# Kernel tuning notes

Measured on AMD Instinct MI355X. Metric: run time of the kernel, lower is better.

Reference implementation:

```python
import jax, jax.numpy as jnp
import numpy as np

B, L, D = 16, 2048, 1024
S = 32                      # spans per example
WIDTH_BUCKET, LEN_BUCKET = 16, 32
NUM_BUCKETS = 64
NUM_LABELS = 3


def setup_inputs() -> dict:
    key = jax.random.key(0)
    k1, k2, k3, k4, k5, k6 = jax.random.split(key, 6)
    encoder_layer = jax.random.normal(k1, (B, L, D), dtype=jnp.float32)
    # variable sequence lengths in [1024, 2048]
    lengths = jax.random.randint(k2, (B,), 1024, L + 1)
    attention_mask = (jnp.arange(L)[None, :] < lengths[:, None]).astype(jnp.int32)
    # non-overlapping spans of width 64: pooled region is [head+1, tail), never empty
    span_head_idxs = jnp.broadcast_to(jnp.arange(S, dtype=jnp.int32) * 64, (B, S))
    span_tail_idxs = span_head_idxs + 64
    labels = jax.random.randint(k3, (B, S), 0, NUM_LABELS, dtype=jnp.int32)
    width_emb = jax.random.normal(k4, (NUM_BUCKETS, 8), dtype=jnp.float32) * 0.02
    length_emb = jax.random.normal(k5, (NUM_BUCKETS, 8), dtype=jnp.float32) * 0.02
    cls_w = jax.random.normal(k6, (D + 16, NUM_LABELS), dtype=jnp.float32) * 0.02
    cls_b = jnp.zeros((NUM_LABELS,), dtype=jnp.float32)
    return {
        "encoder_layer": encoder_layer,
        "attention_mask": attention_mask,
        "span_head_idxs": span_head_idxs,
        "span_tail_idxs": span_tail_idxs,
        "labels": labels,
        "width_emb": width_emb,
        "length_emb": length_emb,
        "cls_w": cls_w,
        "cls_b": cls_b,
    }


def reference(encoder_layer, attention_mask, span_head_idxs, span_tail_idxs,
              labels, width_emb, length_emb, cls_w, cls_b):
    b, l, d = encoder_layer.shape
    s = span_head_idxs.shape[1]
    pos = jnp.arange(l, dtype=jnp.int32)  # [L]
    # ragged span mean: mean over encoder_layer[i, head+1 : tail]
    in_span = (pos[None, None, :] >= span_head_idxs[:, :, None] + 1) & \
              (pos[None, None, :] < span_tail_idxs[:, :, None])           # [B,S,L]
    m = in_span.astype(encoder_layer.dtype)
    counts = jnp.maximum(m.sum(-1, keepdims=True), 1.0)                   # [B,S,1]
    span_mean = jnp.einsum('bsl,bld->bsd', m, encoder_layer) / counts     # [B,S,D]
    # width bucket embedding
    w_bucket = jnp.clip((span_tail_idxs - span_head_idxs) // WIDTH_BUCKET, 0, NUM_BUCKETS - 1)
    width_vec = width_emb[w_bucket]                                       # [B,S,8]
    # length bucket embedding (per-example, broadcast over spans)
    lengths = attention_mask.sum(1)                                       # [B]
    l_bucket = jnp.clip(lengths // LEN_BUCKET, 0, NUM_BUCKETS - 1)
    length_vec = jnp.broadcast_to(length_emb[l_bucket][:, None, :], (b, s, length_emb.shape[1]))
    feat = jnp.concatenate([span_mean, width_vec, length_vec], axis=-1)   # [B,S,D+16]
    # dropout is identity in eval mode
    logits = feat @ cls_w + cls_b                                         # [B,S,num_labels]
    # cross-entropy with ignore_index=-1
    logp = jax.nn.log_softmax(logits, axis=-1).reshape(-1, logits.shape[-1])
    lab = labels.reshape(-1)
    valid = lab > -1
    nll = -jnp.take_along_axis(logp, jnp.clip(lab, 0)[:, None], axis=1)[:, 0]
    ce_loss = jnp.sum(jnp.where(valid, nll, 0.0)) / jnp.maximum(valid.sum(), 1)
    return logits, ce_loss
```

## Files before the change

### kernel.cpp

```cpp
#include <hip/hip_runtime.h>
#include <hip/hip_bf16.h>

#define B_ 16
#define L_ 2048
#define D_ 1024
#define S_ 32

__global__ __launch_bounds__(256) void lengths_kernel(const int* __restrict__ mask,
                                                      int* __restrict__ lbuck) {
    const int b = blockIdx.x;
    const int t = threadIdx.x;
    int s = 0;
    for (int i = t; i < L_; i += 256) s += mask[b * L_ + i];
#pragma unroll
    for (int off = 32; off > 0; off >>= 1) s += __shfl_down(s, off, 64);
    __shared__ int red[4];
    if ((t & 63) == 0) red[t >> 6] = s;
    __syncthreads();
    if (t == 0) {
        int tot = red[0] + red[1] + red[2] + red[3];
        int lb = tot / 32;
        if (lb < 0) lb = 0;
        if (lb > 63) lb = 63;
        lbuck[b] = lb;
    }
}

__global__ __launch_bounds__(256) void span_logits_kernel(
        const float* __restrict__ enc,
        const int* __restrict__ head,
        const int* __restrict__ tail,
        const float* __restrict__ wemb,
        const float* __restrict__ lemb,
        const float* __restrict__ cls_w,
        const float* __restrict__ cls_b,
        const int* __restrict__ lbuck,
        float* __restrict__ out) {
    const int bs = blockIdx.x;
    const int b  = bs / S_;
    const int t  = threadIdx.x;
    const int h  = head[bs];
    const int tl = tail[bs];
    int lo = h + 1; if (lo < 0) lo = 0;
    int hi = tl;    if (hi > L_) hi = L_;
    const int nrow = hi - lo;

    const int dc = t * 4;

    float w00 = cls_w[(dc + 0) * 3 + 0], w01 = cls_w[(dc + 0) * 3 + 1], w02 = cls_w[(dc + 0) * 3 + 2];
    float w10 = cls_w[(dc + 1) * 3 + 0], w11 = cls_w[(dc + 1) * 3 + 1], w12 = cls_w[(dc + 1) * 3 + 2];
    float w20 = cls_w[(dc + 2) * 3 + 0], w21 = cls_w[(dc + 2) * 3 + 1], w22 = cls_w[(dc + 2) * 3 + 2];
    float w30 = cls_w[(dc + 3) * 3 + 0], w31 = cls_w[(dc + 3) * 3 + 1], w32 = cls_w[(dc + 3) * 3 + 2];

    float a0 = 0.f, a1 = 0.f, a2 = 0.f;
    const float* base = enc + (size_t)b * (L_ * D_) + dc;
    for (int l = lo; l < hi; ++l) {
        const float4 u = *reinterpret_cast<const float4*>(base + (size_t)l * D_);
        a0 = fmaf(u.x, w00, a0); a1 = fmaf(u.x, w01, a1); a2 = fmaf(u.x, w02, a2);
        a0 = fmaf(u.y, w10, a0); a1 = fmaf(u.y, w11, a1); a2 = fmaf(u.y, w12, a2);
        a0 = fmaf(u.z, w20, a0); a1 = fmaf(u.z, w21, a1); a2 = fmaf(u.z, w22, a2);
        a0 = fmaf(u.w, w30, a0); a1 = fmaf(u.w, w31, a1); a2 = fmaf(u.w, w32, a2);
    }

#pragma unroll
    for (int off = 32; off > 0; off >>= 1) {
        a0 += __shfl_down(a0, off, 64);
        a1 += __shfl_down(a1, off, 64);
        a2 += __shfl_down(a2, off, 64);
    }
    __shared__ float sred[12];
    const int wv = t >> 6;
    if ((t & 63) == 0) { sred[wv * 3 + 0] = a0; sred[wv * 3 + 1] = a1; sred[wv * 3 + 2] = a2; }
    __syncthreads();

    if (t == 0) {
        float r0 = sred[0] + sred[3] + sred[6] + sred[9];
        float r1 = sred[1] + sred[4] + sred[7] + sred[10];
        float r2 = sred[2] + sred[5] + sred[8] + sred[11];
        float cnt = (float)(nrow > 0 ? nrow : 0);
        if (cnt < 1.f) cnt = 1.f;
        const float inv = 1.f / cnt;
        r0 *= inv; r1 *= inv; r2 *= inv;

        int wb = (tl - h) / 16;
        if (wb < 0) wb = 0;
        if (wb > 63) wb = 63;
        const int lb = lbuck[b];
        const float* we = wemb + wb * 8;
        const float* le = lemb + lb * 8;
#pragma unroll
        for (int j = 0; j < 8; ++j) {
            const float wvf = we[j];
            const float lvf = le[j];
            r0 += wvf * cls_w[(D_ + j) * 3 + 0] + lvf * cls_w[(D_ + 8 + j) * 3 + 0];
            r1 += wvf * cls_w[(D_ + j) * 3 + 1] + lvf * cls_w[(D_ + 8 + j) * 3 + 1];
            r2 += wvf * cls_w[(D_ + j) * 3 + 2] + lvf * cls_w[(D_ + 8 + j) * 3 + 2];
        }
        r0 += cls_b[0];
        r1 += cls_b[1];
        r2 += cls_b[2];

        out[bs * 3 + 0] = r0;
        out[bs * 3 + 1] = r1;
        out[bs * 3 + 2] = r2;
    }
}

__global__ __launch_bounds__(512) void ce_kernel(const float* __restrict__ logits,
                                                 const int* __restrict__ labels,
                                                 float* __restrict__ out) {
    const int i = threadIdx.x;
    const int lab = labels[i];
    const float l0 = logits[i * 3 + 0];
    const float l1 = logits[i * 3 + 1];
    const float l2 = logits[i * 3 + 2];
    const float m  = fmaxf(l0, fmaxf(l1, l2));
    const float lse = m + logf(expf(l0 - m) + expf(l1 - m) + expf(l2 - m));
    int cl = lab < 0 ? 0 : (lab > 2 ? 2 : lab);
    const float pick = (cl == 0) ? l0 : ((cl == 1) ? l1 : l2);
    float nll = 0.f, val = 0.f;
    if (lab > -1) { nll = lse - pick; val = 1.f; }
#pragma unroll
    for (int off = 32; off > 0; off >>= 1) {
        nll += __shfl_down(nll, off, 64);
        val += __shfl_down(val, off, 64);
    }
    __shared__ float rn[8], rv[8];
    const int wv = i >> 6;
    if ((i & 63) == 0) { rn[wv] = nll; rv[wv] = val; }
    __syncthreads();
    if (i == 0) {
        float sn = 0.f, sv = 0.f;
#pragma unroll
        for (int k = 0; k < 8; ++k) { sn += rn[k]; sv += rv[k]; }
        out[B_ * S_ * 3] = sn / fmaxf(sv, 1.f);
    }
}

extern "C" void kernel_launch(void* const* d_in, const int* in_sizes, int n_in,
                              void* d_out, int out_size, void* d_ws, size_t ws_size,
                              hipStream_t stream) {
    const float* enc    = (const float*)d_in[0];
    const int*   mask   = (const int*)d_in[1];
    const int*   head   = (const int*)d_in[2];
    const int*   tail   = (const int*)d_in[3];
    const int*   labels = (const int*)d_in[4];
    const float* wemb   = (const float*)d_in[5];
    const float* lemb   = (const float*)d_in[6];
    const float* cls_w  = (const float*)d_in[7];
    const float* cls_b  = (const float*)d_in[8];
    float* out = (float*)d_out;

    int* lbuck = (int*)d_ws;

    lengths_kernel<<<B_, 256, 0, stream>>>(mask, lbuck);
    span_logits_kernel<<<B_ * S_, 256, 0, stream>>>(enc, head, tail, wemb, lemb,
                                                    cls_w, cls_b, lbuck, out);
    ce_kernel<<<1, 512, 0, stream>>>(out, labels, out);
}
```

Measured before the change: 219.0 us.

## Fuse length reduction into span kernel and split span rows across four thread groups

Removes the separate lengths kernel: each span block now reads the example's 2048-entry mask as int2 pairs and reduces it alongside the logit partials to get the length bucket. Blocks grow to 1024 threads, and four row groups each stride the span rows by four, which raises memory-level parallelism per block. The cost is redundant mask reads across the 32 spans of each example and a larger cross-wave reduction. Fewer waves fit per CU at this block size.

```diff
diff --git a/kernel.cpp b/kernel.cpp
--- a/kernel.cpp
+++ b/kernel.cpp
@@ -6,35 +6,15 @@
 #define D_ 1024
 #define S_ 32
 
-__global__ __launch_bounds__(256) void lengths_kernel(const int* __restrict__ mask,
-                                                      int* __restrict__ lbuck) {
-    const int b = blockIdx.x;
-    const int t = threadIdx.x;
-    int s = 0;
-    for (int i = t; i < L_; i += 256) s += mask[b * L_ + i];
-#pragma unroll
-    for (int off = 32; off > 0; off >>= 1) s += __shfl_down(s, off, 64);
-    __shared__ int red[4];
-    if ((t & 63) == 0) red[t >> 6] = s;
-    __syncthreads();
-    if (t == 0) {
-        int tot = red[0] + red[1] + red[2] + red[3];
-        int lb = tot / 32;
-        if (lb < 0) lb = 0;
-        if (lb > 63) lb = 63;
-        lbuck[b] = lb;
-    }
-}
-
-__global__ __launch_bounds__(256) void span_logits_kernel(
+__global__ __launch_bounds__(1024) void span_logits_kernel(
         const float* __restrict__ enc,
+        const int* __restrict__ mask,
         const int* __restrict__ head,
         const int* __restrict__ tail,
         const float* __restrict__ wemb,
         const float* __restrict__ lemb,
         const float* __restrict__ cls_w,
         const float* __restrict__ cls_b,
-        const int* __restrict__ lbuck,
         float* __restrict__ out) {
     const int bs = blockIdx.x;
     const int b  = bs / S_;
@@ -45,16 +25,20 @@
     int hi = tl;    if (hi > L_) hi = L_;
     const int nrow = hi - lo;
 
-    const int dc = t * 4;
+    const int rg = t >> 8;
+    const int dc = (t & 255) * 4;
 
-    float w00 = cls_w[(dc + 0) * 3 + 0], w01 = cls_w[(dc + 0) * 3 + 1], w02 = cls_w[(dc + 0) * 3 + 2];
-    float w10 = cls_w[(dc + 1) * 3 + 0], w11 = cls_w[(dc + 1) * 3 + 1], w12 = cls_w[(dc + 1) * 3 + 2];
-    float w20 = cls_w[(dc + 2) * 3 + 0], w21 = cls_w[(dc + 2) * 3 + 1], w22 = cls_w[(dc + 2) * 3 + 2];
-    float w30 = cls_w[(dc + 3) * 3 + 0], w31 = cls_w[(dc + 3) * 3 + 1], w32 = cls_w[(dc + 3) * 3 + 2];
+    const int2 mk = reinterpret_cast<const int2*>(mask + b * L_)[t];
+    int msum = mk.x + mk.y;
+
+    const float w00 = cls_w[(dc + 0) * 3 + 0], w01 = cls_w[(dc + 0) * 3 + 1], w02 = cls_w[(dc + 0) * 3 + 2];
+    const float w10 = cls_w[(dc + 1) * 3 + 0], w11 = cls_w[(dc + 1) * 3 + 1], w12 = cls_w[(dc + 1) * 3 + 2];
+    const float w20 = cls_w[(dc + 2) * 3 + 0], w21 = cls_w[(dc + 2) * 3 + 1], w22 = cls_w[(dc + 2) * 3 + 2];
+    const float w30 = cls_w[(dc + 3) * 3 + 0], w31 = cls_w[(dc + 3) * 3 + 1], w32 = cls_w[(dc + 3) * 3 + 2];
 
     float a0 = 0.f, a1 = 0.f, a2 = 0.f;
     const float* base = enc + (size_t)b * (L_ * D_) + dc;
-    for (int l = lo; l < hi; ++l) {
+    for (int l = lo + rg; l < hi; l += 4) {
         const float4 u = *reinterpret_cast<const float4*>(base + (size_t)l * D_);
         a0 = fmaf(u.x, w00, a0); a1 = fmaf(u.x, w01, a1); a2 = fmaf(u.x, w02, a2);
         a0 = fmaf(u.y, w10, a0); a1 = fmaf(u.y, w11, a1); a2 = fmaf(u.y, w12, a2);
@@ -67,16 +51,29 @@
         a0 += __shfl_down(a0, off, 64);
         a1 += __shfl_down(a1, off, 64);
         a2 += __shfl_down(a2, off, 64);
+        msum += __shfl_down(msum, off, 64);
     }
-    __shared__ float sred[12];
+    __shared__ float sred[16 * 3];
+    __shared__ int   slen[16];
     const int wv = t >> 6;
-    if ((t & 63) == 0) { sred[wv * 3 + 0] = a0; sred[wv * 3 + 1] = a1; sred[wv * 3 + 2] = a2; }
+    if ((t & 63) == 0) {
+        sred[wv * 3 + 0] = a0;
+        sred[wv * 3 + 1] = a1;
+        sred[wv * 3 + 2] = a2;
+        slen[wv] = msum;
+    }
     __syncthreads();
 
     if (t == 0) {
-        float r0 = sred[0] + sred[3] + sred[6] + sred[9];
-        float r1 = sred[1] + sred[4] + sred[7] + sred[10];
-        float r2 = sred[2] + sred[5] + sred[8] + sred[11];
+        float r0 = 0.f, r1 = 0.f, r2 = 0.f;
+        int len = 0;
+#pragma unroll
+        for (int k = 0; k < 16; ++k) {
+            r0 += sred[k * 3 + 0];
+            r1 += sred[k * 3 + 1];
+            r2 += sred[k * 3 + 2];
+            len += slen[k];
+        }
         float cnt = (float)(nrow > 0 ? nrow : 0);
         if (cnt < 1.f) cnt = 1.f;
         const float inv = 1.f / cnt;
@@ -85,7 +82,9 @@
         int wb = (tl - h) / 16;
         if (wb < 0) wb = 0;
         if (wb > 63) wb = 63;
-        const int lb = lbuck[b];
+        int lb = len / 32;
+        if (lb < 0) lb = 0;
+        if (lb > 63) lb = 63;
         const float* we = wemb + wb * 8;
         const float* le = lemb + lb * 8;
 #pragma unroll
@@ -151,10 +150,7 @@
     const float* cls_b  = (const float*)d_in[8];
     float* out = (float*)d_out;
 
-    int* lbuck = (int*)d_ws;
-
-    lengths_kernel<<<B_, 256, 0, stream>>>(mask, lbuck);
-    span_logits_kernel<<<B_ * S_, 256, 0, stream>>>(enc, head, tail, wemb, lemb,
-                                                    cls_w, cls_b, lbuck, out);
+    span_logits_kernel<<<B_ * S_, 1024, 0, stream>>>(enc, mask, head, tail, wemb, lemb,
+                                                     cls_w, cls_b, out);
     ce_kernel<<<1, 512, 0, stream>>>(out, labels, out);
 }
```

New measurement: 206.4 us. 5.8% less time.
